# Optimization experiments

Measured on AMD Instinct MI355X. Metric: run time of the kernel, lower is better.

Reference implementation:

```python
import jax, jax.numpy as jnp
import numpy as np

EPS = 1e-12  # matches torch F.normalize default eps

def setup_inputs() -> dict:
    key = jax.random.key(0)
    k1, k2 = jax.random.split(key)
    n, d = 8192, 1024
    x = jax.random.normal(k1, (n, d), dtype=jnp.float32)
    weight = jax.random.normal(k2, (d, d), dtype=jnp.float32) * (2.0 / d) ** 0.5
    return {"x": x, "weight": weight}

def reference(x, weight):
    # L2-normalize rows (torch F.normalize, dim=1): x / max(||x||_2, eps)
    nrm = jnp.sqrt(jnp.sum(x * x, axis=1, keepdims=True))
    norm = x / jnp.maximum(nrm, EPS)
    # adjacency: cosine-similarity Gram matrix [n, n] (materialized as in source)
    adj = norm @ norm.T
    ax = adj @ x          # [n, d]
    axw = ax @ weight     # [n, d]
    return axw
```

## Files before the change

kernel.cpp:

```cpp
#include <hip/hip_runtime.h>
#include <stdint.h>

typedef unsigned short u16;
typedef unsigned int u32;
typedef __attribute__((ext_vector_type(8))) short short8;
typedef __attribute__((ext_vector_type(4))) float floatx4;

__device__ __forceinline__ u16 f2b(float f) {
    u32 u = __builtin_bit_cast(u32, f);
    return (u16)((u + 0x7fffu + ((u >> 16) & 1u)) >> 16);
}

__device__ __forceinline__ void gld16(const void* g, void* l) {
    __builtin_amdgcn_global_load_lds(
        (const __attribute__((address_space(1))) u32*)g,
        (__attribute__((address_space(3))) u32*)l, 16, 0, 0);
}

__global__ __launch_bounds__(256) void prep_norms(
    const float* __restrict__ x, float* __restrict__ rnorm, float* __restrict__ srnorm) {
    int row = blockIdx.x;
    int t = threadIdx.x;
    float4 v = ((const float4*)(x + (long)row * 1024))[t];
    float ss = v.x * v.x + v.y * v.y + v.z * v.z + v.w * v.w;
    #pragma unroll
    for (int off = 32; off > 0; off >>= 1) ss += __shfl_down(ss, off);
    __shared__ float red[4];
    if ((t & 63) == 0) red[t >> 6] = ss;
    __syncthreads();
    if (t == 0) {
        float r = 1.0f / fmaxf(sqrtf(red[0] + red[1] + red[2] + red[3]), 1e-12f);
        rnorm[row] = r;
        srnorm[row] = sqrtf(r);
    }
}

__global__ __launch_bounds__(256) void transpose_scale(
    const float* __restrict__ src, const float* __restrict__ sr,
    u16* __restrict__ dst, int rows, int cols) {
    __shared__ float tile[64][65];
    __shared__ float rbuf[64];
    int r0 = blockIdx.x * 64, c0 = blockIdx.y * 64;
    int t = threadIdx.x;
    #pragma unroll
    for (int i = 0; i < 4; i++) {
        int lin = i * 256 + t;
        int rr = lin >> 4, c4 = (lin & 15) << 2;
        float4 v = *(const float4*)(src + (long)(r0 + rr) * cols + c0 + c4);
        tile[rr][c4] = v.x; tile[rr][c4 + 1] = v.y; tile[rr][c4 + 2] = v.z; tile[rr][c4 + 3] = v.w;
    }
    if (t < 64) rbuf[t] = (sr != nullptr) ? sr[r0 + t] : 1.0f;
    __syncthreads();
    #pragma unroll
    for (int i = 0; i < 4; i++) {
        int lin = i * 256 + t;
        int cc = lin >> 4, r4 = (lin & 15) << 2;
        ushort4 o;
        o.x = f2b(tile[r4][cc] * rbuf[r4]);
        o.y = f2b(tile[r4 + 1][cc] * rbuf[r4 + 1]);
        o.z = f2b(tile[r4 + 2][cc] * rbuf[r4 + 2]);
        o.w = f2b(tile[r4 + 3][cc] * rbuf[r4 + 3]);
        *(ushort4*)(dst + (long)(c0 + cc) * rows + r0 + r4) = o;
    }
}

__global__ __launch_bounds__(256) void cast_f2b(const float* __restrict__ S, u16* __restrict__ D) {
    long i = ((long)blockIdx.x * 256 + threadIdx.x) * 4;
    float4 v = *(const float4*)(S + i);
    ushort4 o;
    o.x = f2b(v.x); o.y = f2b(v.y); o.z = f2b(v.z); o.w = f2b(v.w);
    *(ushort4*)(D + i) = o;
}

__global__ __launch_bounds__(256) void reduce_cast(
    const float* __restrict__ P, u16* __restrict__ D, int S, long E) {
    long i = ((long)blockIdx.x * 256 + threadIdx.x) * 4;
    float4 s = *(const float4*)(P + i);
    for (int z = 1; z < S; z++) {
        float4 v = *(const float4*)(P + z * E + i);
        s.x += v.x; s.y += v.y; s.z += v.z; s.w += v.w;
    }
    ushort4 o;
    o.x = f2b(s.x); o.y = f2b(s.y); o.z = f2b(s.z); o.w = f2b(s.w);
    *(ushort4*)(D + i) = o;
}

__global__ __launch_bounds__(256, 4) void gemm64x128(
    const u16* __restrict__ A, const u16* __restrict__ B,
    float* __restrict__ C, const float* __restrict__ rowscale,
    int lda, int ldb, int ldc, int tilesN, int kIters, long coffz) {
    __shared__ __align__(16) u16 As[64 * 64];
    __shared__ __align__(16) u16 Bs[128 * 64];
    int bid = blockIdx.x;
    int tm = bid / tilesN, tn = bid % tilesN;
    long kOff = (long)blockIdx.y * kIters * 64;
    const u16* Ap = A + (long)tm * 64 * lda + kOff;
    const u16* Bp = B + (long)tn * 128 * ldb + kOff;
    long coff = (long)blockIdx.y * coffz;

    int t = threadIdx.x;
    int lane = t & 63, w = t >> 6;
    int wm = (w & 1) * 32, wn = (w >> 1) * 64;
    int r16 = lane & 15, q = lane >> 4;

    int acl[2], bcl[4];
    #pragma unroll
    for (int j = 0; j < 2; j++) acl[j] = (w * 2 + j) * 64 + lane;
    #pragma unroll
    for (int j = 0; j < 4; j++) bcl[j] = (w * 4 + j) * 64 + lane;

    floatx4 acc[2][4];
    #pragma unroll
    for (int i = 0; i < 2; i++)
        #pragma unroll
        for (int j = 0; j < 4; j++) acc[i][j] = (floatx4){0.f, 0.f, 0.f, 0.f};

    for (int kt = 0; kt < kIters; kt++) {
        long kk = (long)kt * 64;
        #pragma unroll
        for (int j = 0; j < 2; j++) {
            int cl = acl[j], row = cl >> 3, cg = (cl & 7) ^ (row & 7);
            gld16(Ap + (long)row * lda + kk + cg * 8, (void*)&As[cl * 8]);
        }
        #pragma unroll
        for (int j = 0; j < 4; j++) {
            int cl = bcl[j], row = cl >> 3, cg = (cl & 7) ^ (row & 7);
            gld16(Bp + (long)row * ldb + kk + cg * 8, (void*)&Bs[cl * 8]);
        }
        __syncthreads();
        #pragma unroll
        for (int ks = 0; ks < 2; ks++) {
            short8 a[2], b[4];
            #pragma unroll
            for (int i = 0; i < 2; i++) {
                int r = wm + i * 16 + r16;
                int c = (ks * 4 + q) ^ (r & 7);
                a[i] = *(const short8*)&As[r * 64 + c * 8];
            }
            #pragma unroll
            for (int j = 0; j < 4; j++) {
                int r = wn + j * 16 + r16;
                int c = (ks * 4 + q) ^ (r & 7);
                b[j] = *(const short8*)&Bs[r * 64 + c * 8];
            }
            #pragma unroll
            for (int i = 0; i < 2; i++)
                #pragma unroll
                for (int j = 0; j < 4; j++)
                    acc[i][j] = __builtin_amdgcn_mfma_f32_16x16x32_bf16(a[i], b[j], acc[i][j], 0, 0, 0);
        }
        __syncthreads();
    }

    int m0 = tm * 64 + wm, n0 = tn * 128 + wn;
    #pragma unroll
    for (int i = 0; i < 2; i++) {
        int mm = m0 + i * 16 + q * 4;
        float rs[4];
        #pragma unroll
        for (int r = 0; r < 4; r++) rs[r] = (rowscale != nullptr) ? rowscale[mm + r] : 1.0f;
        #pragma unroll
        for (int j = 0; j < 4; j++) {
            int nn = n0 + j * 16 + r16;
            #pragma unroll
            for (int r = 0; r < 4; r++)
                C[coff + (long)(mm + r) * ldc + nn] = acc[i][j][r] * rs[r];
        }
    }
}

extern "C" void kernel_launch(void* const* d_in, const int* in_sizes, int n_in,
                              void* d_out, int out_size, void* d_ws, size_t ws_size,
                              hipStream_t stream) {
    const float* x = (const float*)d_in[0];
    const float* wgt = (const float*)d_in[1];
    float* out = (float*)d_out;
    char* ws = (char*)d_ws;

    const size_t MB = 1048576;
    float* rnorm  = (float*)ws;
    float* srnorm = (float*)(ws + 32768);
    u16*   YT     = (u16*)(ws + 65536);
    u16*   Wt     = (u16*)(ws + 65536 + 16 * MB);
    u16*   Gb     = (u16*)(ws + 65536 + 18 * MB);
    u16*   Mt     = (u16*)(ws + 65536 + 20 * MB);
    char*  REGION = ws + 65536 + 22 * MB;
    float* Gp     = (float*)REGION;
    u16*   xb     = (u16*)REGION;
    float* Mp     = (float*)(REGION + 16 * MB);

    prep_norms<<<8192, 256, 0, stream>>>(x, rnorm, srnorm);
    transpose_scale<<<dim3(128, 16), 256, 0, stream>>>(x, srnorm, YT, 8192, 1024);
    transpose_scale<<<dim3(16, 16), 256, 0, stream>>>(wgt, nullptr, Wt, 1024, 1024);
    gemm64x128<<<dim3(128, 8), 256, 0, stream>>>(YT, YT, Gp, nullptr,
                                                 8192, 8192, 1024, 8, 16, 1048576);
    reduce_cast<<<1024, 256, 0, stream>>>(Gp, Gb, 8, 1048576);
    cast_f2b<<<8192, 256, 0, stream>>>(x, xb);
    gemm64x128<<<dim3(128, 2), 256, 0, stream>>>(Wt, Gb, Mp, nullptr,
                                                 1024, 1024, 1024, 8, 8, 1048576);
    reduce_cast<<<1024, 256, 0, stream>>>(Mp, Mt, 2, 1048576);
    gemm64x128<<<dim3(1024, 1), 256, 0, stream>>>(xb, Mt, out, rnorm,
                                                  1024, 1024, 1024, 8, 16, 0);
}
```

Measured before the change: 177.0 us.

## Exploit Gram symmetry to compute only lower tiles and fuse x cast into transpose

```diff
diff --git a/kernel.cpp b/kernel.cpp
--- a/kernel.cpp
+++ b/kernel.cpp
@@ -35,41 +35,40 @@
     }
 }
 
-__global__ __launch_bounds__(256) void transpose_scale(
+__global__ __launch_bounds__(256) void transpose_scale_dual(
     const float* __restrict__ src, const float* __restrict__ sr,
-    u16* __restrict__ dst, int rows, int cols) {
+    u16* __restrict__ dstT, u16* __restrict__ dstR, int rows, int cols) {
     __shared__ float tile[64][65];
     __shared__ float rbuf[64];
     int r0 = blockIdx.x * 64, c0 = blockIdx.y * 64;
     int t = threadIdx.x;
+    if (t < 64) rbuf[t] = (sr != nullptr) ? sr[r0 + t] : 1.0f;
+    __syncthreads();
     #pragma unroll
     for (int i = 0; i < 4; i++) {
         int lin = i * 256 + t;
         int rr = lin >> 4, c4 = (lin & 15) << 2;
         float4 v = *(const float4*)(src + (long)(r0 + rr) * cols + c0 + c4);
+        float s = rbuf[rr];
+        v.x *= s; v.y *= s; v.z *= s; v.w *= s;
         tile[rr][c4] = v.x; tile[rr][c4 + 1] = v.y; tile[rr][c4 + 2] = v.z; tile[rr][c4 + 3] = v.w;
-    }
-    if (t < 64) rbuf[t] = (sr != nullptr) ? sr[r0 + t] : 1.0f;
+        if (dstR != nullptr) {
+            ushort4 o; o.x = f2b(v.x); o.y = f2b(v.y); o.z = f2b(v.z); o.w = f2b(v.w);
+            *(ushort4*)(dstR + (long)(r0 + rr) * cols + c0 + c4) = o;
+        }
+    }
     __syncthreads();
     #pragma unroll
     for (int i = 0; i < 4; i++) {
         int lin = i * 256 + t;
         int cc = lin >> 4, r4 = (lin & 15) << 2;
         ushort4 o;
-        o.x = f2b(tile[r4][cc] * rbuf[r4]);
-        o.y = f2b(tile[r4 + 1][cc] * rbuf[r4 + 1]);
-        o.z = f2b(tile[r4 + 2][cc] * rbuf[r4 + 2]);
-        o.w = f2b(tile[r4 + 3][cc] * rbuf[r4 + 3]);
-        *(ushort4*)(dst + (long)(c0 + cc) * rows + r0 + r4) = o;
-    }
-}
-
-__global__ __launch_bounds__(256) void cast_f2b(const float* __restrict__ S, u16* __restrict__ D) {
-    long i = ((long)blockIdx.x * 256 + threadIdx.x) * 4;
-    float4 v = *(const float4*)(S + i);
-    ushort4 o;
-    o.x = f2b(v.x); o.y = f2b(v.y); o.z = f2b(v.z); o.w = f2b(v.w);
-    *(ushort4*)(D + i) = o;
+        o.x = f2b(tile[r4][cc]);
+        o.y = f2b(tile[r4 + 1][cc]);
+        o.z = f2b(tile[r4 + 2][cc]);
+        o.w = f2b(tile[r4 + 3][cc]);
+        *(ushort4*)(dstT + (long)(c0 + cc) * rows + r0 + r4) = o;
+    }
 }
 
 __global__ __launch_bounds__(256) void reduce_cast(
@@ -85,14 +84,68 @@
     *(ushort4*)(D + i) = o;
 }
 
+__global__ __launch_bounds__(256) void reduce_sym64(
+    const float* __restrict__ P, u16* __restrict__ D, int S, long E) {
+    __shared__ float lt[64][65];
+    int ti = blockIdx.x >> 4, tj = blockIdx.x & 15;
+    int t = threadIdx.x;
+    int r = t >> 4, c4 = (t & 15) << 2;
+    int kept = (ti <= 2 * (tj >> 1) + 1);
+    if (kept) {
+        #pragma unroll
+        for (int it = 0; it < 4; it++) {
+            int row = 64 * ti + it * 16 + r;
+            long idx = (long)row * 1024 + 64 * tj + c4;
+            float4 s = *(const float4*)(P + idx);
+            for (int z = 1; z < S; z++) {
+                float4 v = *(const float4*)(P + (long)z * E + idx);
+                s.x += v.x; s.y += v.y; s.z += v.z; s.w += v.w;
+            }
+            ushort4 o; o.x = f2b(s.x); o.y = f2b(s.y); o.z = f2b(s.z); o.w = f2b(s.w);
+            *(ushort4*)(D + idx) = o;
+        }
+    } else {
+        #pragma unroll
+        for (int it = 0; it < 4; it++) {
+            int row = it * 16 + r;
+            long idx = (long)(64 * tj + row) * 1024 + 64 * ti + c4;
+            float4 s = *(const float4*)(P + idx);
+            for (int z = 1; z < S; z++) {
+                float4 v = *(const float4*)(P + (long)z * E + idx);
+                s.x += v.x; s.y += v.y; s.z += v.z; s.w += v.w;
+            }
+            lt[row][c4] = s.x; lt[row][c4 + 1] = s.y; lt[row][c4 + 2] = s.z; lt[row][c4 + 3] = s.w;
+        }
+        __syncthreads();
+        #pragma unroll
+        for (int it = 0; it < 4; it++) {
+            int dr = it * 16 + r;
+            ushort4 o;
+            o.x = f2b(lt[c4 + 0][dr]); o.y = f2b(lt[c4 + 1][dr]);
+            o.z = f2b(lt[c4 + 2][dr]); o.w = f2b(lt[c4 + 3][dr]);
+            *(ushort4*)(D + (long)(64 * ti + dr) * 1024 + 64 * tj + c4) = o;
+        }
+    }
+}
+
 __global__ __launch_bounds__(256, 4) void gemm64x128(
     const u16* __restrict__ A, const u16* __restrict__ B,
     float* __restrict__ C, const float* __restrict__ rowscale,
-    int lda, int ldb, int ldc, int tilesN, int kIters, long coffz) {
+    int lda, int ldb, int ldc, int tilesN, int kIters, long coffz, int sym) {
     __shared__ __align__(16) u16 As[64 * 64];
     __shared__ __align__(16) u16 Bs[128 * 64];
-    int bid = blockIdx.x;
-    int tm = bid / tilesN, tn = bid % tilesN;
+    int tm, tn;
+    if (sym) {
+        int id = blockIdx.x, j = 0;
+        while (true) {
+            int c = (2 * j + 2 < 16) ? (2 * j + 2) : 16;
+            if (id < c) break;
+            id -= c; j++;
+        }
+        tn = j; tm = id;
+    } else {
+        tm = blockIdx.x / tilesN; tn = blockIdx.x % tilesN;
+    }
     long kOff = (long)blockIdx.y * kIters * 64;
     const u16* Ap = A + (long)tm * 64 * lda + kOff;
     const u16* Bp = B + (long)tn * 128 * ldb + kOff;
@@ -133,15 +186,15 @@
             short8 a[2], b[4];
             #pragma unroll
             for (int i = 0; i < 2; i++) {
-                int r = wm + i * 16 + r16;
-                int c = (ks * 4 + q) ^ (r & 7);
-                a[i] = *(const short8*)&As[r * 64 + c * 8];
+                int rr = wm + i * 16 + r16;
+                int cc = (ks * 4 + q) ^ (rr & 7);
+                a[i] = *(const short8*)&As[rr * 64 + cc * 8];
             }
             #pragma unroll
             for (int j = 0; j < 4; j++) {
-                int r = wn + j * 16 + r16;
-                int c = (ks * 4 + q) ^ (r & 7);
-                b[j] = *(const short8*)&Bs[r * 64 + c * 8];
+                int rr = wn + j * 16 + r16;
+                int cc = (ks * 4 + q) ^ (rr & 7);
+                b[j] = *(const short8*)&Bs[rr * 64 + cc * 8];
             }
             #pragma unroll
             for (int i = 0; i < 2; i++)
@@ -181,24 +234,22 @@
     float* rnorm  = (float*)ws;
     float* srnorm = (float*)(ws + 32768);
     u16*   YT     = (u16*)(ws + 65536);
-    u16*   Wt     = (u16*)(ws + 65536 + 16 * MB);
-    u16*   Gb     = (u16*)(ws + 65536 + 18 * MB);
-    u16*   Mt     = (u16*)(ws + 65536 + 20 * MB);
-    char*  REGION = ws + 65536 + 22 * MB;
-    float* Gp     = (float*)REGION;
-    u16*   xb     = (u16*)REGION;
-    float* Mp     = (float*)(REGION + 16 * MB);
+    u16*   Yb     = (u16*)(ws + 65536 + 16 * MB);
+    u16*   Wt     = (u16*)(ws + 65536 + 32 * MB);
+    u16*   Gb     = (u16*)(ws + 65536 + 34 * MB);
+    u16*   Mt     = (u16*)(ws + 65536 + 36 * MB);
+    float* Gp     = (float*)(ws + 65536 + 38 * MB);
+    float* Mp     = (float*)(ws + 65536 + 70 * MB);
 
     prep_norms<<<8192, 256, 0, stream>>>(x, rnorm, srnorm);
-    transpose_scale<<<dim3(128, 16), 256, 0, stream>>>(x, srnorm, YT, 8192, 1024);
-    transpose_scale<<<dim3(16, 16), 256, 0, stream>>>(wgt, nullptr, Wt, 1024, 1024);
-    gemm64x128<<<dim3(128, 8), 256, 0, stream>>>(YT, YT, Gp, nullptr,
-                                                 8192, 8192, 1024, 8, 16, 1048576);
-    reduce_cast<<<1024, 256, 0, stream>>>(Gp, Gb, 8, 1048576);
-    cast_f2b<<<8192, 256, 0, stream>>>(x, xb);
+    transpose_scale_dual<<<dim3(128, 16), 256, 0, stream>>>(x, srnorm, YT, Yb, 8192, 1024);
+    transpose_scale_dual<<<dim3(16, 16), 256, 0, stream>>>(wgt, nullptr, Wt, nullptr, 1024, 1024);
+    gemm64x128<<<dim3(72, 8), 256, 0, stream>>>(YT, YT, Gp, nullptr,
+                                                8192, 8192, 1024, 8, 16, 1048576, 1);
+    reduce_sym64<<<256, 256, 0, stream>>>(Gp, Gb, 8, 1048576);
     gemm64x128<<<dim3(128, 2), 256, 0, stream>>>(Wt, Gb, Mp, nullptr,
-                                                 1024, 1024, 1024, 8, 8, 1048576);
+                                                 1024, 1024, 1024, 8, 8, 1048576, 0);
     reduce_cast<<<1024, 256, 0, stream>>>(Mp, Mt, 2, 1048576);
-    gemm64x128<<<dim3(1024, 1), 256, 0, stream>>>(xb, Mt, out, rnorm,
-                                                  1024, 1024, 1024, 8, 16, 0);
-}
+    gemm64x128<<<dim3(1024, 1), 256, 0, stream>>>(Yb, Mt, out, srnorm,
+                                                  1024, 1024, 1024, 8, 16, 0, 0);
+}
```

Result: faster. 167.6 us (-5.3%).
